# Performance work log

Hardware: AMD Instinct MI355X
Metric: run time of the kernel (lower is better)

## Reference

```python
import jax, jax.numpy as jnp
import numpy as np


def _mlp(x, W1, b1, W2, b2):
    # x: [..., 3d]; Linear weights stored torch-style: W1 [d, 3d], W2 [1, d]
    h = jax.nn.relu(jnp.einsum('...i,di->...d', x, W1) + b1)
    return jax.nn.sigmoid(jnp.einsum('...d,od->...o', h, W2) + b2)[..., 0]


def setup_inputs() -> dict:
    key = jax.random.key(0)
    ks = jax.random.split(key, 6)
    N, d, E, K = 1000000, 64, 65536, 16
    embeds = jax.random.normal(ks[0], (N, d), dtype=jnp.float32)
    pos = jax.random.randint(ks[1], (E, 2), 0, N, dtype=jnp.int64)
    neg = jax.random.randint(ks[2], (E, K, 2), 0, N, dtype=jnp.int64)
    # xavier-uniform init as in the torch module
    lim1 = float(np.sqrt(6.0 / (3 * d + d)))
    lim2 = float(np.sqrt(6.0 / (d + 1)))
    W1 = jax.random.uniform(ks[3], (d, 3 * d), jnp.float32, -lim1, lim1)
    b1 = jnp.zeros((d,), jnp.float32)
    W2 = jax.random.uniform(ks[4], (1, d), jnp.float32, -lim2, lim2)
    b2 = jnp.zeros((1,), jnp.float32)
    return {"embeds": embeds, "pos": pos, "neg": neg,
            "W1": W1, "b1": b1, "W2": W2, "b2": b2}


def reference(embeds, pos, neg, W1, b1, W2, b2):
    # positive pairs: [E, 3d]
    pu = embeds[pos[:, 0]]
    pv = embeds[pos[:, 1]]
    pos_emb = jnp.concatenate([pu, pv, pu * pv], axis=-1)
    # negative pairs: [E, K, 3d]
    nu = embeds[neg[:, :, 0]]
    nv = embeds[neg[:, :, 1]]
    neg_emb = jnp.concatenate([nu, nv, nu * nv], axis=-1)
    pos_scr = jnp.exp(_mlp(pos_emb, W1, b1, W2, b2))          # [E]
    neg_scr = jnp.exp(_mlp(neg_emb, W1, b1, W2, b2))          # [E, K]
    denom = jnp.sum(neg_scr, axis=-1) + pos_scr               # [E]
    loss = -jnp.sum(pos_scr / (denom + 1e-8) + 1e-8)
    return loss
```

## Files before the change

### kernel.cpp

```cpp
#include <hip/hip_runtime.h>
#include <hip/hip_fp16.h>
#include <math.h>

#define N_EMB   1000000
#define D       64
#define E_PAIRS 65536
#define K_NEG   16
#define P_TOTAL (E_PAIRS * (K_NEG + 1))
#define PPB     128

typedef __attribute__((ext_vector_type(8))) short     short8;
typedef __attribute__((ext_vector_type(8))) _Float16  half8;
typedef __attribute__((ext_vector_type(4))) float     float4v;


static __device__ __forceinline__ unsigned short f2bf(float f) {
    unsigned int x = __float_as_uint(f);
    unsigned int r = (x + 0x7fffu + ((x >> 16) & 1u)) >> 16;
    return (unsigned short)r;
}

static __device__ __forceinline__ unsigned int h2mul(unsigned int a, unsigned int b) {
    union { unsigned int u; __half2 h; } A, B, R;
    A.u = a; B.u = b;
    R.h = __hmul2(A.h, B.h);
    return R.u;
}

static __device__ __forceinline__ uint4 h2mul4(uint4 a, uint4 b) {
    return make_uint4(h2mul(a.x, b.x), h2mul(a.y, b.y),
                      h2mul(a.z, b.z), h2mul(a.w, b.w));
}

static __device__ __forceinline__ float4v mfma16f(uint4 a, uint4 b, float4v c) {
    union { uint4 u; half8 h; } A, B;
    A.u = a; B.u = b;
    return __builtin_amdgcn_mfma_f32_16x16x32_f16(A.h, B.h, c, 0, 0, 0);
}


__global__ __launch_bounds__(256)
void prep_f16(const float* __restrict__ embeds, const float* __restrict__ W1,
              __half* __restrict__ emb16, __half* __restrict__ W1h)
{
    const int nchunks = N_EMB * D / 8;
    const int stride  = gridDim.x * blockDim.x;
    for (int c = blockIdx.x * blockDim.x + threadIdx.x; c < nchunks; c += stride) {
        const float4v* src = (const float4v*)embeds + (size_t)c * 2;
        float4v f0 = __builtin_nontemporal_load(src);
        float4v f1 = __builtin_nontemporal_load(src + 1);
        union { unsigned short s[8]; uint4 u; } o;
        o.s[0] = __half_as_ushort(__float2half(f0[0]));
        o.s[1] = __half_as_ushort(__float2half(f0[1]));
        o.s[2] = __half_as_ushort(__float2half(f0[2]));
        o.s[3] = __half_as_ushort(__float2half(f0[3]));
        o.s[4] = __half_as_ushort(__float2half(f1[0]));
        o.s[5] = __half_as_ushort(__float2half(f1[1]));
        o.s[6] = __half_as_ushort(__float2half(f1[2]));
        o.s[7] = __half_as_ushort(__float2half(f1[3]));
        *((uint4*)emb16 + c) = o.u;
    }
    if (blockIdx.x == 0)
        for (int i = threadIdx.x; i < 64 * 192; i += 256)
            W1h[i] = __float2half(W1[i]);
}

__global__ __launch_bounds__(256, 4)
void score_f16(const __half* __restrict__ emb,
               const int*    __restrict__ pos,
               const int*    __restrict__ neg,
               const __half* __restrict__ W1h,
               const float*  __restrict__ b1,
               const float*  __restrict__ W2,
               const float*  __restrict__ b2,
               float*        __restrict__ scores)
{
    const int t    = threadIdx.x;
    const int lane = t & 63;
    const int wave = t >> 6;
    const int c16  = lane & 15;
    const int quad = lane >> 4;
    const int pw   = blockIdx.x * PPB + wave * 32;

    const int p0 = pw + c16;
    const int p1 = pw + 16 + c16;
    int2 i0, i1;
    if (pw < E_PAIRS) {
        i0 = ((const int2*)pos)[p0];
        i1 = ((const int2*)pos)[p1];
    } else {
        i0 = ((const int2*)neg)[p0 - E_PAIRS];
        i1 = ((const int2*)neg)[p1 - E_PAIRS];
    }

    const __half* u0p = emb + (long long)i0.x * D + quad * 8;
    const __half* v0p = emb + (long long)i0.y * D + quad * 8;
    const __half* u1p = emb + (long long)i1.x * D + quad * 8;
    const __half* v1p = emb + (long long)i1.y * D + quad * 8;

    uint4 a0[6], a1[6];
    a0[0] = *(const uint4*)(u0p);
    a0[1] = *(const uint4*)(u0p + 32);
    a0[2] = *(const uint4*)(v0p);
    a0[3] = *(const uint4*)(v0p + 32);
    a1[0] = *(const uint4*)(u1p);
    a1[1] = *(const uint4*)(u1p + 32);
    a1[2] = *(const uint4*)(v1p);
    a1[3] = *(const uint4*)(v1p + 32);
    a0[4] = h2mul4(a0[0], a0[2]);
    a0[5] = h2mul4(a0[1], a0[3]);
    a1[4] = h2mul4(a1[0], a1[2]);
    a1[5] = h2mul4(a1[1], a1[3]);

    float4v acc[2][4];
    #pragma unroll
    for (int mt = 0; mt < 2; ++mt)
        #pragma unroll
        for (int nt = 0; nt < 4; ++nt)
            acc[mt][nt] = (float4v){0.f, 0.f, 0.f, 0.f};

    #pragma unroll
    for (int ks = 0; ks < 6; ++ks) {
        const int koff = ks * 32 + quad * 8;
        uint4 bfrag[4];
        #pragma unroll
        for (int nt = 0; nt < 4; ++nt)
            bfrag[nt] = *(const uint4*)(W1h + (nt * 16 + c16) * 192 + koff);
        #pragma unroll
        for (int nt = 0; nt < 4; ++nt) {
            acc[0][nt] = mfma16f(a0[ks], bfrag[nt], acc[0][nt]);
            acc[1][nt] = mfma16f(a1[ks], bfrag[nt], acc[1][nt]);
        }
    }

    float b1v[4], w2v[4];
    #pragma unroll
    for (int nt = 0; nt < 4; ++nt) {
        b1v[nt] = b1[nt * 16 + c16];
        w2v[nt] = W2[nt * 16 + c16];
    }
    const float b2v = b2[0];

    #pragma unroll
    for (int mt = 0; mt < 2; ++mt) {
        #pragma unroll
        for (int reg = 0; reg < 4; ++reg) {
            float s = 0.f;
            #pragma unroll
            for (int nt = 0; nt < 4; ++nt) {
                float h = acc[mt][nt][reg] + b1v[nt];
                s += (h > 0.f ? h : 0.f) * w2v[nt];
            }
            s += __shfl_xor(s, 1);
            s += __shfl_xor(s, 2);
            s += __shfl_xor(s, 4);
            s += __shfl_xor(s, 8);
            if (c16 == 0) {
                float sig = 1.f / (1.f + expf(-(s + b2v)));
                scores[pw + mt * 16 + quad * 4 + reg] = expf(sig);
            }
        }
    }
}


static __device__ __forceinline__ short8 pack8(float4 a, float4 b) {
    short8 r;
    r[0] = (short)f2bf(a.x); r[1] = (short)f2bf(a.y);
    r[2] = (short)f2bf(a.z); r[3] = (short)f2bf(a.w);
    r[4] = (short)f2bf(b.x); r[5] = (short)f2bf(b.y);
    r[6] = (short)f2bf(b.z); r[7] = (short)f2bf(b.w);
    return r;
}
static __device__ __forceinline__ float4 mul4(float4 a, float4 b) {
    return make_float4(a.x * b.x, a.y * b.y, a.z * b.z, a.w * b.w);
}
static __device__ __forceinline__ void load_frags(const float* __restrict__ embeds,
                                                  int ui, int vi, int quad, short8* fr)
{
    const float* up = embeds + (long long)ui * D + quad * 8;
    const float* vp = embeds + (long long)vi * D + quad * 8;
    float4 ua = *(const float4*)(up);
    float4 ub = *(const float4*)(up + 4);
    float4 uc = *(const float4*)(up + 32);
    float4 ud = *(const float4*)(up + 36);
    float4 va = *(const float4*)(vp);
    float4 vb = *(const float4*)(vp + 4);
    float4 vc = *(const float4*)(vp + 32);
    float4 vd = *(const float4*)(vp + 36);
    fr[0] = pack8(ua, ub); fr[1] = pack8(uc, ud);
    fr[2] = pack8(va, vb); fr[3] = pack8(vc, vd);
    fr[4] = pack8(mul4(ua, va), mul4(ub, vb));
    fr[5] = pack8(mul4(uc, vc), mul4(ud, vd));
}

__global__ __launch_bounds__(256)
void prep_w1bf(const float* __restrict__ W1, unsigned short* __restrict__ W1bf)
{
    int i = blockIdx.x * 256 + threadIdx.x;
    if (i < 64 * 192) W1bf[i] = f2bf(W1[i]);
}

__global__ __launch_bounds__(256, 4)
void score_f32(const float* __restrict__ embeds,
               const int*   __restrict__ pos,
               const int*   __restrict__ neg,
               const unsigned short* __restrict__ W1bf,
               const float* __restrict__ b1,
               const float* __restrict__ W2,
               const float* __restrict__ b2,
               float*       __restrict__ scores)
{
    const int t    = threadIdx.x;
    const int lane = t & 63;
    const int wave = t >> 6;
    const int c16  = lane & 15;
    const int quad = lane >> 4;
    const int pw   = blockIdx.x * PPB + wave * 32;

    const int p0 = pw + c16;
    const int p1 = pw + 16 + c16;
    int2 i0, i1;
    if (pw < E_PAIRS) {
        i0 = ((const int2*)pos)[p0];
        i1 = ((const int2*)pos)[p1];
    } else {
        i0 = ((const int2*)neg)[p0 - E_PAIRS];
        i1 = ((const int2*)neg)[p1 - E_PAIRS];
    }

    short8 a0[6], a1[6];
    load_frags(embeds, i0.x, i0.y, quad, a0);
    load_frags(embeds, i1.x, i1.y, quad, a1);

    float4v acc[2][4];
    #pragma unroll
    for (int mt = 0; mt < 2; ++mt)
        #pragma unroll
        for (int nt = 0; nt < 4; ++nt)
            acc[mt][nt] = (float4v){0.f, 0.f, 0.f, 0.f};

    #pragma unroll
    for (int ks = 0; ks < 6; ++ks) {
        const int koff = ks * 32 + quad * 8;
        short8 bfrag[4];
        #pragma unroll
        for (int nt = 0; nt < 4; ++nt)
            bfrag[nt] = *(const short8*)(W1bf + (nt * 16 + c16) * 192 + koff);
        #pragma unroll
        for (int nt = 0; nt < 4; ++nt) {
            acc[0][nt] = __builtin_amdgcn_mfma_f32_16x16x32_bf16(a0[ks], bfrag[nt], acc[0][nt], 0, 0, 0);
            acc[1][nt] = __builtin_amdgcn_mfma_f32_16x16x32_bf16(a1[ks], bfrag[nt], acc[1][nt], 0, 0, 0);
        }
    }

    float b1v[4], w2v[4];
    #pragma unroll
    for (int nt = 0; nt < 4; ++nt) {
        b1v[nt] = b1[nt * 16 + c16];
        w2v[nt] = W2[nt * 16 + c16];
    }
    const float b2v = b2[0];

    #pragma unroll
    for (int mt = 0; mt < 2; ++mt) {
        #pragma unroll
        for (int reg = 0; reg < 4; ++reg) {
            float s = 0.f;
            #pragma unroll
            for (int nt = 0; nt < 4; ++nt) {
                float h = acc[mt][nt][reg] + b1v[nt];
                s += (h > 0.f ? h : 0.f) * w2v[nt];
            }
            s += __shfl_xor(s, 1);
            s += __shfl_xor(s, 2);
            s += __shfl_xor(s, 4);
            s += __shfl_xor(s, 8);
            if (c16 == 0) {
                float sig = 1.f / (1.f + expf(-(s + b2v)));
                scores[pw + mt * 16 + quad * 4 + reg] = expf(sig);
            }
        }
    }
}


__global__ __launch_bounds__(256)
void reduce_atomic(const float* __restrict__ scores, float* __restrict__ out)
{
    __shared__ float sdata[256];
    int e = blockIdx.x * 256 + threadIdx.x;
    float pos_s = scores[e];
    const float* ns = scores + E_PAIRS + (size_t)e * K_NEG;
    float nsum = 0.f;
    #pragma unroll
    for (int c = 0; c < 4; ++c) {
        float4 v = *(const float4*)(ns + c * 4);
        nsum += v.x + v.y + v.z + v.w;
    }
    float term = pos_s / (pos_s + nsum + 1e-8f) + 1e-8f;
    sdata[threadIdx.x] = term;
    __syncthreads();
    for (int s = 128; s > 0; s >>= 1) {
        if (threadIdx.x < s) sdata[threadIdx.x] += sdata[threadIdx.x + s];
        __syncthreads();
    }
    if (threadIdx.x == 0) atomicAdd(out, -sdata[0]);
}


extern "C" void kernel_launch(void* const* d_in, const int* in_sizes, int n_in,
                              void* d_out, int out_size, void* d_ws, size_t ws_size,
                              hipStream_t stream)
{
    const float* embeds = (const float*)d_in[0];
    const int*   pos    = (const int*)d_in[1];
    const int*   neg    = (const int*)d_in[2];
    const float* W1     = (const float*)d_in[3];
    const float* b1     = (const float*)d_in[4];
    const float* W2     = (const float*)d_in[5];
    const float* b2     = (const float*)d_in[6];
    float* out = (float*)d_out;

    const size_t EMB16_BYTES = (size_t)N_EMB * D * 2;
    const size_t need = EMB16_BYTES + (size_t)P_TOTAL * 4 + 64 * 192 * 2;

    (void)hipMemsetAsync(out, 0, sizeof(float), stream);

    if (ws_size >= need) {
        __half* emb16  = (__half*)d_ws;
        float*  scores = (float*)((char*)d_ws + EMB16_BYTES);
        __half* W1h    = (__half*)(scores + P_TOTAL);

        prep_f16<<<4096, 256, 0, stream>>>(embeds, W1, emb16, W1h);
        score_f16<<<P_TOTAL / PPB, 256, 0, stream>>>(emb16, pos, neg, W1h, b1, W2, b2, scores);
        reduce_atomic<<<E_PAIRS / 256, 256, 0, stream>>>(scores, out);
    } else {
        float* scores = (float*)d_ws;
        unsigned short* W1bf = (unsigned short*)(scores + P_TOTAL);

        prep_w1bf<<<48, 256, 0, stream>>>(W1, W1bf);
        score_f32<<<P_TOTAL / PPB, 256, 0, stream>>>(embeds, pos, neg, W1bf, b1, W2, b2, scores);
        reduce_atomic<<<E_PAIRS / 256, 256, 0, stream>>>(scores, out);
    }
}
```

Baseline: 493.7 us.

## Stage W1 in padded LDS and software-pipeline gathers across four groups per wave

The f16 scoring kernel now copies W1 into shared memory once per block, padding rows to 200 halves to reduce bank conflicts. Each wave processes four 32-pair groups and double-buffers the embedding gathers, so the loads for the next group are in flight while MFMAs run on the current one. Launch bounds drop to 3 blocks per CU to make room for the extra registers, and the grid is a quarter of its former size. The aim is to hide gather latency and avoid re-reading W1 from global/L2 in every wave. The costs are lower occupancy and a per-block LDS fill plus barrier.

```diff
diff --git a/kernel.cpp b/kernel.cpp
--- a/kernel.cpp
+++ b/kernel.cpp
@@ -7,7 +7,10 @@
 #define E_PAIRS 65536
 #define K_NEG   16
 #define P_TOTAL (E_PAIRS * (K_NEG + 1))
-#define PPB     128
+#define NGROUPS (P_TOTAL / 32)
+#define GPW     4
+#define SCORE_BLOCKS (NGROUPS / (4 * GPW))
+#define W1S     200
 
 typedef __attribute__((ext_vector_type(8))) short     short8;
 typedef __attribute__((ext_vector_type(8))) _Float16  half8;
@@ -65,7 +68,77 @@
             W1h[i] = __float2half(W1[i]);
 }
 
-__global__ __launch_bounds__(256, 4)
+
+#define LOADIDX(gg, ii0, ii1) do {                                        \
+    int _p0 = (gg) * 32 + c16;                                            \
+    if ((gg) < E_PAIRS / 32) {                                            \
+        ii0 = ((const int2*)pos)[_p0];                                    \
+        ii1 = ((const int2*)pos)[_p0 + 16];                               \
+    } else {                                                              \
+        ii0 = ((const int2*)neg)[_p0 - E_PAIRS];                          \
+        ii1 = ((const int2*)neg)[_p0 + 16 - E_PAIRS];                     \
+    }                                                                     \
+} while (0)
+
+#define GATHER8(ii0, ii1, BUF) do {                                       \
+    const __half* _u0 = emb + (long long)(ii0).x * D + quad * 8;          \
+    const __half* _v0 = emb + (long long)(ii0).y * D + quad * 8;          \
+    const __half* _u1 = emb + (long long)(ii1).x * D + quad * 8;          \
+    const __half* _v1 = emb + (long long)(ii1).y * D + quad * 8;          \
+    BUF##0 = *(const uint4*)(_u0);      BUF##1 = *(const uint4*)(_u0+32); \
+    BUF##2 = *(const uint4*)(_v0);      BUF##3 = *(const uint4*)(_v0+32); \
+    BUF##4 = *(const uint4*)(_u1);      BUF##5 = *(const uint4*)(_u1+32); \
+    BUF##6 = *(const uint4*)(_v1);      BUF##7 = *(const uint4*)(_v1+32); \
+} while (0)
+
+#define COMPUTE_GROUP(BUF, gg) do {                                       \
+    uint4 a0[6], a1[6];                                                   \
+    a0[0]=BUF##0; a0[1]=BUF##1; a0[2]=BUF##2; a0[3]=BUF##3;               \
+    a1[0]=BUF##4; a1[1]=BUF##5; a1[2]=BUF##6; a1[3]=BUF##7;               \
+    a0[4]=h2mul4(a0[0],a0[2]); a0[5]=h2mul4(a0[1],a0[3]);                 \
+    a1[4]=h2mul4(a1[0],a1[2]); a1[5]=h2mul4(a1[1],a1[3]);                 \
+    float4v acc[2][4];                                                    \
+    _Pragma("unroll")                                                     \
+    for (int mt = 0; mt < 2; ++mt)                                        \
+        _Pragma("unroll")                                                 \
+        for (int nt = 0; nt < 4; ++nt)                                    \
+            acc[mt][nt] = (float4v){0.f, 0.f, 0.f, 0.f};                  \
+    _Pragma("unroll")                                                     \
+    for (int ks = 0; ks < 6; ++ks) {                                      \
+        const int koff = ks * 32 + quad * 8;                              \
+        uint4 bfrag[4];                                                   \
+        _Pragma("unroll")                                                 \
+        for (int nt = 0; nt < 4; ++nt)                                    \
+            bfrag[nt] = *(const uint4*)(&w1s[(nt*16 + c16)*W1S + koff]);  \
+        _Pragma("unroll")                                                 \
+        for (int nt = 0; nt < 4; ++nt) {                                  \
+            acc[0][nt] = mfma16f(a0[ks], bfrag[nt], acc[0][nt]);          \
+            acc[1][nt] = mfma16f(a1[ks], bfrag[nt], acc[1][nt]);          \
+        }                                                                 \
+    }                                                                     \
+    _Pragma("unroll")                                                     \
+    for (int mt = 0; mt < 2; ++mt) {                                      \
+        _Pragma("unroll")                                                 \
+        for (int reg = 0; reg < 4; ++reg) {                               \
+            float s = 0.f;                                                \
+            _Pragma("unroll")                                             \
+            for (int nt = 0; nt < 4; ++nt) {                              \
+                float h = acc[mt][nt][reg] + b1v[nt];                     \
+                s += (h > 0.f ? h : 0.f) * w2v[nt];                       \
+            }                                                             \
+            s += __shfl_xor(s, 1);                                        \
+            s += __shfl_xor(s, 2);                                        \
+            s += __shfl_xor(s, 4);                                        \
+            s += __shfl_xor(s, 8);                                        \
+            if (c16 == 0) {                                               \
+                float sig = 1.f / (1.f + expf(-(s + b2v)));               \
+                scores[(gg)*32 + mt*16 + quad*4 + reg] = expf(sig);       \
+            }                                                             \
+        }                                                                 \
+    }                                                                     \
+} while (0)
+
+__global__ __launch_bounds__(256, 3)
 void score_f16(const __half* __restrict__ emb,
                const int*    __restrict__ pos,
                const int*    __restrict__ neg,
@@ -75,12 +148,103 @@
                const float*  __restrict__ b2,
                float*        __restrict__ scores)
 {
+    __shared__ __half w1s[64 * W1S];
+
     const int t    = threadIdx.x;
     const int lane = t & 63;
     const int wave = t >> 6;
     const int c16  = lane & 15;
     const int quad = lane >> 4;
-    const int pw   = blockIdx.x * PPB + wave * 32;
+
+    for (int idx = t * 8; idx < 64 * 192; idx += 256 * 8) {
+        int n = idx / 192, k = idx - n * 192;
+        *(uint4*)(&w1s[n * W1S + k]) = *(const uint4*)(W1h + idx);
+    }
+    __syncthreads();
+
+    float b1v[4], w2v[4];
+    #pragma unroll
+    for (int nt = 0; nt < 4; ++nt) {
+        b1v[nt] = b1[nt * 16 + c16];
+        w2v[nt] = W2[nt * 16 + c16];
+    }
+    const float b2v = b2[0];
+
+    const int gw = blockIdx.x * 4 + wave;
+    const int g0 = gw * GPW;
+
+    int2 ia0, ib0, ia1, ib1, ia2, ib2, ia3, ib3;
+    uint4 A0, A1, A2, A3, A4, A5, A6, A7;
+    uint4 B0, B1, B2, B3, B4, B5, B6, B7;
+
+    LOADIDX(g0 + 0, ia0, ib0);
+    LOADIDX(g0 + 1, ia1, ib1);
+    GATHER8(ia0, ib0, A);
+    GATHER8(ia1, ib1, B);
+    LOADIDX(g0 + 2, ia2, ib2);
+    COMPUTE_GROUP(A, g0 + 0);
+    GATHER8(ia2, ib2, A);
+    LOADIDX(g0 + 3, ia3, ib3);
+    COMPUTE_GROUP(B, g0 + 1);
+    GATHER8(ia3, ib3, B);
+    COMPUTE_GROUP(A, g0 + 2);
+    COMPUTE_GROUP(B, g0 + 3);
+}
+
+
+static __device__ __forceinline__ short8 pack8(float4 a, float4 b) {
+    short8 r;
+    r[0] = (short)f2bf(a.x); r[1] = (short)f2bf(a.y);
+    r[2] = (short)f2bf(a.z); r[3] = (short)f2bf(a.w);
+    r[4] = (short)f2bf(b.x); r[5] = (short)f2bf(b.y);
+    r[6] = (short)f2bf(b.z); r[7] = (short)f2bf(b.w);
+    return r;
+}
+static __device__ __forceinline__ float4 mul4(float4 a, float4 b) {
+    return make_float4(a.x * b.x, a.y * b.y, a.z * b.z, a.w * b.w);
+}
+static __device__ __forceinline__ void load_frags(const float* __restrict__ embeds,
+                                                  int ui, int vi, int quad, short8* fr)
+{
+    const float* up = embeds + (long long)ui * D + quad * 8;
+    const float* vp = embeds + (long long)vi * D + quad * 8;
+    float4 ua = *(const float4*)(up);
+    float4 ub = *(const float4*)(up + 4);
+    float4 uc = *(const float4*)(up + 32);
+    float4 ud = *(const float4*)(up + 36);
+    float4 va = *(const float4*)(vp);
+    float4 vb = *(const float4*)(vp + 4);
+    float4 vc = *(const float4*)(vp + 32);
+    float4 vd = *(const float4*)(vp + 36);
+    fr[0] = pack8(ua, ub); fr[1] = pack8(uc, ud);
+    fr[2] = pack8(va, vb); fr[3] = pack8(vc, vd);
+    fr[4] = pack8(mul4(ua, va), mul4(ub, vb));
+    fr[5] = pack8(mul4(uc, vc), mul4(ud, vd));
+}
+
+__global__ __launch_bounds__(256)
+void prep_w1bf(const float* __restrict__ W1, unsigned short* __restrict__ W1bf)
+{
+    int i = blockIdx.x * 256 + threadIdx.x;
+    if (i < 64 * 192) W1bf[i] = f2bf(W1[i]);
+}
+
+__global__ __launch_bounds__(256, 4)
+void score_f32(const float* __restrict__ embeds,
+               const int*   __restrict__ pos,
+               const int*   __restrict__ neg,
+               const unsigned short* __restrict__ W1bf,
+               const float* __restrict__ b1,
+               const float* __restrict__ W2,
+               const float* __restrict__ b2,
+               float*       __restrict__ scores)
+{
+    const int t    = threadIdx.x;
+    const int lane = t & 63;
+    const int wave = t >> 6;
+    const int c16  = lane & 15;
+    const int quad = lane >> 4;
+    const int pw   = blockIdx.x * 128 + wave * 32;
 
     const int p0 = pw + c16;
     const int p1 = pw + 16 + c16;
@@ -93,24 +257,9 @@
         i1 = ((const int2*)neg)[p1 - E_PAIRS];
     }
 
-    const __half* u0p = emb + (long long)i0.x * D + quad * 8;
-    const __half* v0p = emb + (long long)i0.y * D + quad * 8;
-    const __half* u1p = emb + (long long)i1.x * D + quad * 8;
-    const __half* v1p = emb + (long long)i1.y * D + quad * 8;
-
-    uint4 a0[6], a1[6];
-    a0[0] = *(const uint4*)(u0p);
-    a0[1] = *(const uint4*)(u0p + 32);
-    a0[2] = *(const uint4*)(v0p);
-    a0[3] = *(const uint4*)(v0p + 32);
-    a1[0] = *(const uint4*)(u1p);
-    a1[1] = *(const uint4*)(u1p + 32);
-    a1[2] = *(const uint4*)(v1p);
-    a1[3] = *(const uint4*)(v1p + 32);
-    a0[4] = h2mul4(a0[0], a0[2]);
-    a0[5] = h2mul4(a0[1], a0[3]);
-    a1[4] = h2mul4(a1[0], a1[2]);
-    a1[5] = h2mul4(a1[1], a1[3]);
+    short8 a0[6], a1[6];
+    load_frags(embeds, i0.x, i0.y, quad, a0);
+    load_frags(embeds, i1.x, i1.y, quad, a1);
 
     float4v acc[2][4];
     #pragma unroll
@@ -122,14 +271,14 @@
     #pragma unroll
     for (int ks = 0; ks < 6; ++ks) {
         const int koff = ks * 32 + quad * 8;
-        uint4 bfrag[4];
+        short8 bfrag[4];
         #pragma unroll
         for (int nt = 0; nt < 4; ++nt)
-            bfrag[nt] = *(const uint4*)(W1h + (nt * 16 + c16) * 192 + koff);
+            bfrag[nt] = *(const short8*)(W1bf + (nt * 16 + c16) * 192 + koff);
         #pragma unroll
         for (int nt = 0; nt < 4; ++nt) {
-            acc[0][nt] = mfma16f(a0[ks], bfrag[nt], acc[0][nt]);
-            acc[1][nt] = mfma16f(a1[ks], bfrag[nt], acc[1][nt]);
+            acc[0][nt] = __builtin_amdgcn_mfma_f32_16x16x32_bf16(a0[ks], bfrag[nt], acc[0][nt], 0, 0, 0);
+            acc[1][nt] = __builtin_amdgcn_mfma_f32_16x16x32_bf16(a1[ks], bfrag[nt], acc[1][nt], 0, 0, 0);
         }
     }
 
@@ -164,127 +313,6 @@
 }
 
 
-static __device__ __forceinline__ short8 pack8(float4 a, float4 b) {
-    short8 r;
-    r[0] = (short)f2bf(a.x); r[1] = (short)f2bf(a.y);
-    r[2] = (short)f2bf(a.z); r[3] = (short)f2bf(a.w);
-    r[4] = (short)f2bf(b.x); r[5] = (short)f2bf(b.y);
-    r[6] = (short)f2bf(b.z); r[7] = (short)f2bf(b.w);
-    return r;
-}
-static __device__ __forceinline__ float4 mul4(float4 a, float4 b) {
-    return make_float4(a.x * b.x, a.y * b.y, a.z * b.z, a.w * b.w);
-}
-static __device__ __forceinline__ void load_frags(const float* __restrict__ embeds,
-                                                  int ui, int vi, int quad, short8* fr)
-{
-    const float* up = embeds + (long long)ui * D + quad * 8;
-    const float* vp = embeds + (long long)vi * D + quad * 8;
-    float4 ua = *(const float4*)(up);
-    float4 ub = *(const float4*)(up + 4);
-    float4 uc = *(const float4*)(up + 32);
-    float4 ud = *(const float4*)(up + 36);
-    float4 va = *(const float4*)(vp);
-    float4 vb = *(const float4*)(vp + 4);
-    float4 vc = *(const float4*)(vp + 32);
-    float4 vd = *(const float4*)(vp + 36);
-    fr[0] = pack8(ua, ub); fr[1] = pack8(uc, ud);
-    fr[2] = pack8(va, vb); fr[3] = pack8(vc, vd);
-    fr[4] = pack8(mul4(ua, va), mul4(ub, vb));
-    fr[5] = pack8(mul4(uc, vc), mul4(ud, vd));
-}
-
-__global__ __launch_bounds__(256)
-void prep_w1bf(const float* __restrict__ W1, unsigned short* __restrict__ W1bf)
-{
-    int i = blockIdx.x * 256 + threadIdx.x;
-    if (i < 64 * 192) W1bf[i] = f2bf(W1[i]);
-}
-
-__global__ __launch_bounds__(256, 4)
-void score_f32(const float* __restrict__ embeds,
-               const int*   __restrict__ pos,
-               const int*   __restrict__ neg,
-               const unsigned short* __restrict__ W1bf,
-               const float* __restrict__ b1,
-               const float* __restrict__ W2,
-               const float* __restrict__ b2,
-               float*       __restrict__ scores)
-{
-    const int t    = threadIdx.x;
-    const int lane = t & 63;
-    const int wave = t >> 6;
-    const int c16  = lane & 15;
-    const int quad = lane >> 4;
-    const int pw   = blockIdx.x * PPB + wave * 32;
-
-    const int p0 = pw + c16;
-    const int p1 = pw + 16 + c16;
-    int2 i0, i1;
-    if (pw < E_PAIRS) {
-        i0 = ((const int2*)pos)[p0];
-        i1 = ((const int2*)pos)[p1];
-    } else {
-        i0 = ((const int2*)neg)[p0 - E_PAIRS];
-        i1 = ((const int2*)neg)[p1 - E_PAIRS];
-    }
-
-    short8 a0[6], a1[6];
-    load_frags(embeds, i0.x, i0.y, quad, a0);
-    load_frags(embeds, i1.x, i1.y, quad, a1);
-
-    float4v acc[2][4];
-    #pragma unroll
-    for (int mt = 0; mt < 2; ++mt)
-        #pragma unroll
-        for (int nt = 0; nt < 4; ++nt)
-            acc[mt][nt] = (float4v){0.f, 0.f, 0.f, 0.f};
-
-    #pragma unroll
-    for (int ks = 0; ks < 6; ++ks) {
-        const int koff = ks * 32 + quad * 8;
-        short8 bfrag[4];
-        #pragma unroll
-        for (int nt = 0; nt < 4; ++nt)
-            bfrag[nt] = *(const short8*)(W1bf + (nt * 16 + c16) * 192 + koff);
-        #pragma unroll
-        for (int nt = 0; nt < 4; ++nt) {
-            acc[0][nt] = __builtin_amdgcn_mfma_f32_16x16x32_bf16(a0[ks], bfrag[nt], acc[0][nt], 0, 0, 0);
-            acc[1][nt] = __builtin_amdgcn_mfma_f32_16x16x32_bf16(a1[ks], bfrag[nt], acc[1][nt], 0, 0, 0);
-        }
-    }
-
-    float b1v[4], w2v[4];
-    #pragma unroll
-    for (int nt = 0; nt < 4; ++nt) {
-        b1v[nt] = b1[nt * 16 + c16];
-        w2v[nt] = W2[nt * 16 + c16];
-    }
-    const float b2v = b2[0];
-
-    #pragma unroll
-    for (int mt = 0; mt < 2; ++mt) {
-        #pragma unroll
-        for (int reg = 0; reg < 4; ++reg) {
-            float s = 0.f;
-            #pragma unroll
-            for (int nt = 0; nt < 4; ++nt) {
-                float h = acc[mt][nt][reg] + b1v[nt];
-                s += (h > 0.f ? h : 0.f) * w2v[nt];
-            }
-            s += __shfl_xor(s, 1);
-            s += __shfl_xor(s, 2);
-            s += __shfl_xor(s, 4);
-            s += __shfl_xor(s, 8);
-            if (c16 == 0) {
-                float sig = 1.f / (1.f + expf(-(s + b2v)));
-                scores[pw + mt * 16 + quad * 4 + reg] = expf(sig);
-            }
-        }
-    }
-}
-
-
 __global__ __launch_bounds__(256)
 void reduce_atomic(const float* __restrict__ scores, float* __restrict__ out)
 {
@@ -333,14 +361,14 @@
         __half* W1h    = (__half*)(scores + P_TOTAL);
 
         prep_f16<<<4096, 256, 0, stream>>>(embeds, W1, emb16, W1h);
-        score_f16<<<P_TOTAL / PPB, 256, 0, stream>>>(emb16, pos, neg, W1h, b1, W2, b2, scores);
+        score_f16<<<SCORE_BLOCKS, 256, 0, stream>>>(emb16, pos, neg, W1h, b1, W2, b2, scores);
         reduce_atomic<<<E_PAIRS / 256, 256, 0, stream>>>(scores, out);
     } else {
         float* scores = (float*)d_ws;
         unsigned short* W1bf = (unsigned short*)(scores + P_TOTAL);
 
         prep_w1bf<<<48, 256, 0, stream>>>(W1, W1bf);
-        score_f32<<<P_TOTAL / PPB, 256, 0, stream>>>(embeds, pos, neg, W1bf, b1, W2, b2, scores);
+        score_f32<<<P_TOTAL / 128, 256, 0, stream>>>(embeds, pos, neg, W1bf, b1, W2, b2, scores);
         reduce_atomic<<<E_PAIRS / 256, 256, 0, stream>>>(scores, out);
     }
 }
```

Measured after the change: 430.5 us. -12.8%, faster.
